# Optimization experiments

Hardware: AMD Instinct MI355X
Metric: run time of the kernel (lower is better)

Reference implementation:

```python
import jax, jax.numpy as jnp
import numpy as np
from jax import lax

WS = 8   # window size
NH = 8   # num heads
EPS = 1e-5  # BatchNorm eps (eval mode, running mean=0 var=1)

def _rel_pos_index(ws):
    coords = np.stack(np.meshgrid(np.arange(ws), np.arange(ws), indexing='ij'))
    cf = coords.reshape(2, -1)
    rel = (cf[:, :, None] - cf[:, None, :]).transpose(1, 2, 0).astype(np.int64)
    rel[..., 0] += ws - 1
    rel[..., 1] += ws - 1
    rel[..., 0] *= 2 * ws - 1
    return rel.sum(-1)  # [ws*ws, ws*ws]

REL_IDX = _rel_pos_index(WS)

def conv2d(x, w, b=None, pad=0, groups=1):
    y = lax.conv_general_dilated(x, w, (1, 1), [(pad, pad), (pad, pad)],
                                 dimension_numbers=('NCHW', 'OIHW', 'NCHW'),
                                 feature_group_count=groups)
    if b is not None:
        y = y + b[None, :, None, None]
    return y

def bn(x, g, b):
    # eval-mode BatchNorm with running_mean=0, running_var=1
    scale = g / np.float32(np.sqrt(1.0 + EPS))
    return x * scale[None, :, None, None] + b[None, :, None, None]

def avgpool(x, kh, kw, ph, pw):
    # PyTorch AvgPool2d: zero padding, count_include_pad=True -> divide by kernel size
    s = lax.reduce_window(x, 0.0, lax.add, (1, 1, kh, kw), (1, 1, 1, 1),
                          [(0, 0), (0, 0), (ph, ph), (pw, pw)])
    return s / (kh * kw)

def setup_inputs() -> dict:
    key = jax.random.key(0)
    ks = jax.random.split(key, 8)
    C = 256
    x = jax.random.normal(ks[0], (8, C, 128, 128), dtype=jnp.float32)
    qkv_w = jax.random.normal(ks[1], (3 * C, C, 1, 1), dtype=jnp.float32) * 0.05
    qkv_b = jnp.zeros((3 * C,), jnp.float32)
    local_w = jax.random.normal(ks[2], (C, C // NH, 3, 3), dtype=jnp.float32) * 0.05
    local_b = jnp.zeros((C,), jnp.float32)
    rpb_table = jax.random.normal(ks[3], ((2 * WS - 1) ** 2, NH), dtype=jnp.float32) * 0.02
    proj_dw_w = jax.random.normal(ks[4], (C, 1, 3, 3), dtype=jnp.float32) * 0.05
    proj_dw_b = jnp.zeros((C,), jnp.float32)
    proj_pw_w = jax.random.normal(ks[5], (C, C, 1, 1), dtype=jnp.float32) * 0.05
    proj_pw_b = jnp.zeros((C,), jnp.float32)
    return {
        'x': x, 'qkv_w': qkv_w, 'qkv_b': qkv_b,
        'local_w': local_w, 'local_b': local_b,
        'local_bn_g': jnp.ones((C,), jnp.float32), 'local_bn_b': jnp.zeros((C,), jnp.float32),
        'rpb_table': rpb_table,
        'proj_dw_w': proj_dw_w, 'proj_dw_b': proj_dw_b,
        'proj_bn_g': jnp.ones((C,), jnp.float32), 'proj_bn_b': jnp.zeros((C,), jnp.float32),
        'proj_pw_w': proj_pw_w, 'proj_pw_b': proj_pw_b,
    }

def reference(x, qkv_w, qkv_b, local_w, local_b, local_bn_g, local_bn_b,
              rpb_table, proj_dw_w, proj_dw_b, proj_bn_g, proj_bn_b,
              proj_pw_w, proj_pw_b):
    B, C, H, W = x.shape
    hd = C // NH
    scale = hd ** -0.5
    # local branch: grouped 3x3 conv (groups=num_heads) + BN + ReLU
    local = jax.nn.relu(bn(conv2d(x, local_w, local_b, pad=1, groups=NH),
                           local_bn_g, local_bn_b))
    # H, W divisible by WS -> self.pad (reflect) is a no-op
    qkv = conv2d(x, qkv_w, qkv_b)  # [B, 3C, H, W]
    Hh, Ww = H // WS, W // WS
    # 'b (qkv h d) (hh ws1) (ww ws2) -> qkv (b hh ww) h (ws1 ws2) d'
    qkv = qkv.reshape(B, 3, NH, hd, Hh, WS, Ww, WS)
    qkv = qkv.transpose(1, 0, 4, 6, 2, 5, 7, 3).reshape(3, B * Hh * Ww, NH, WS * WS, hd)
    q, k, v = qkv[0], qkv[1], qkv[2]
    dots = jnp.einsum('bhid,bhjd->bhij', q, k) * scale  # [Bwin, NH, 64, 64]
    bias = rpb_table[REL_IDX.reshape(-1)].reshape(WS * WS, WS * WS, NH).transpose(2, 0, 1)
    attn = jax.nn.softmax(dots + bias[None], axis=-1)
    out = jnp.einsum('bhij,bhjd->bhid', attn, v)
    # '(b hh ww) h (ws1 ws2) d -> b (h d) (hh ws1) (ww ws2)'
    out = out.reshape(B, Hh, Ww, NH, WS, WS, hd).transpose(0, 3, 6, 1, 4, 2, 5).reshape(B, C, H, W)
    # asymmetric avg-pool fusion with reflect pre-pad
    ax = avgpool(jnp.pad(out, ((0, 0), (0, 0), (0, 1), (0, 0)), mode='reflect'),
                 WS, 1, WS // 2 - 1, 0)
    ay = avgpool(jnp.pad(out, ((0, 0), (0, 0), (0, 0), (0, 1)), mode='reflect'),
                 1, WS, 0, WS // 2 - 1)
    out = ax + ay + local
    # pad_out: reflect (0,1,0,1)
    out = jnp.pad(out, ((0, 0), (0, 0), (0, 1), (0, 1)), mode='reflect')
    # SeparableConvBN proj: depthwise 3x3 -> BN -> pointwise 1x1
    out = conv2d(out, proj_dw_w, proj_dw_b, pad=1, groups=C)
    out = bn(out, proj_bn_g, proj_bn_b)
    out = conv2d(out, proj_pw_w, proj_pw_b)
    return out[:, :, :H, :W]
```

## Files before the change

### kernel.cpp

```cpp
#include <hip/hip_runtime.h>
#include <cstddef>

#define C_ 256
#define H_ 128
#define W_ 128
#define HW_ 16384
#define NH_ 8
#define NWIN_ 256
#define EPS_ 1e-5f

typedef short s16x8 __attribute__((ext_vector_type(8)));
typedef float f32x4 __attribute__((ext_vector_type(4)));

__device__ inline void bf16_split(float f, short& h, short& l) {
  unsigned u = __float_as_uint(f);
  unsigned hb = (u + 0x7FFFu + ((u >> 16) & 1u)) >> 16;
  float hf = __uint_as_float(hb << 16);
  h = (short)hb;
  float r = f - hf;
  unsigned v = __float_as_uint(r);
  unsigned lb = (v + 0x7FFFu + ((v >> 16) & 1u)) >> 16;
  l = (short)lb;
}

__global__ __launch_bounds__(256) void k1_qkv_mfma(
    const float* __restrict__ xb, const float* __restrict__ wq,
    const float* __restrict__ bias, float* __restrict__ qkv_s) {
  __shared__ short s_a[2][128][40];
  __shared__ short s_b[2][128][40];
  const int tid = threadIdx.x;
  const int y   = blockIdx.x;
  const int oc0 = blockIdx.y * 128;

  const int lane = tid & 63;
  const int wid  = tid >> 6;
  const int m0w = (wid >> 1) * 64;
  const int n0w = (wid & 1) * 64;

  f32x4 acc[4][4];
#pragma unroll
  for (int i = 0; i < 4; ++i)
#pragma unroll
    for (int j = 0; j < 4; ++j) acc[i][j] = f32x4{0.f, 0.f, 0.f, 0.f};

  const int pcol = tid & 127;
  const int kq0  = tid >> 7;

  for (int k0 = 0; k0 < 256; k0 += 32) {
#pragma unroll
    for (int i = 0; i < 4; ++i) {
      const int ff = tid + i * 256;
      const int row = ff >> 3;
      const int c4 = ff & 7;
      const float4 w4 = *reinterpret_cast<const float4*>(
          &wq[(size_t)(oc0 + row) * 256 + k0 + c4 * 4]);
      short h0, h1, h2, h3, l0, l1, l2, l3;
      bf16_split(w4.x, h0, l0);
      bf16_split(w4.y, h1, l1);
      bf16_split(w4.z, h2, l2);
      bf16_split(w4.w, h3, l3);
      *reinterpret_cast<short4*>(&s_a[0][row][c4 * 4]) = make_short4(h0, h1, h2, h3);
      *reinterpret_cast<short4*>(&s_a[1][row][c4 * 4]) = make_short4(l0, l1, l2, l3);
    }
#pragma unroll
    for (int it = 0; it < 4; ++it) {
      const int kq = kq0 * 4 + it;
      short h[4], l[4];
#pragma unroll
      for (int e = 0; e < 4; ++e) {
        const float v = xb[(size_t)(k0 + kq * 4 + e) * HW_ + y * W_ + pcol];
        bf16_split(v, h[e], l[e]);
      }
      *reinterpret_cast<short4*>(&s_b[0][pcol][kq * 4]) = make_short4(h[0], h[1], h[2], h[3]);
      *reinterpret_cast<short4*>(&s_b[1][pcol][kq * 4]) = make_short4(l[0], l[1], l[2], l[3]);
    }
    __syncthreads();

    const int mr = lane & 15;
    const int kg = (lane >> 4) * 8;
    s16x8 ah[4], al[4], bh[4], bl[4];
#pragma unroll
    for (int fm = 0; fm < 4; ++fm) {
      ah[fm] = *reinterpret_cast<const s16x8*>(&s_a[0][m0w + fm * 16 + mr][kg]);
      al[fm] = *reinterpret_cast<const s16x8*>(&s_a[1][m0w + fm * 16 + mr][kg]);
    }
#pragma unroll
    for (int fn = 0; fn < 4; ++fn) {
      bh[fn] = *reinterpret_cast<const s16x8*>(&s_b[0][n0w + fn * 16 + mr][kg]);
      bl[fn] = *reinterpret_cast<const s16x8*>(&s_b[1][n0w + fn * 16 + mr][kg]);
    }
#pragma unroll
    for (int fm = 0; fm < 4; ++fm)
#pragma unroll
      for (int fn = 0; fn < 4; ++fn) {
        acc[fm][fn] = __builtin_amdgcn_mfma_f32_16x16x32_bf16(
            ah[fm], bh[fn], acc[fm][fn], 0, 0, 0);
        acc[fm][fn] = __builtin_amdgcn_mfma_f32_16x16x32_bf16(
            ah[fm], bl[fn], acc[fm][fn], 0, 0, 0);
        acc[fm][fn] = __builtin_amdgcn_mfma_f32_16x16x32_bf16(
            al[fm], bh[fn], acc[fm][fn], 0, 0, 0);
      }
    __syncthreads();
  }

  const int mr4 = (lane >> 4) * 4;
  const int nn  = lane & 15;
  const int hh = y >> 3, ws1 = y & 7;
#pragma unroll
  for (int fm = 0; fm < 4; ++fm) {
    const int oc = oc0 + m0w + fm * 16 + mr4;
    const float4 b4 = *reinterpret_cast<const float4*>(&bias[oc]);
    const int qkvi = oc >> 8;
    const int head = (oc >> 5) & 7;
    const int d0 = oc & 31;
#pragma unroll
    for (int fn = 0; fn < 4; ++fn) {
      const int x = n0w + fn * 16 + nn;
      const int win = hh * 16 + (x >> 3);
      const int pos = ws1 * 8 + (x & 7);
      const size_t addr =
          ((((size_t)qkvi * NWIN_ + win) * NH_ + head) * 64 + pos) * 32 + d0;
      float4 v;
      v.x = acc[fm][fn].x + b4.x;
      v.y = acc[fm][fn].y + b4.y;
      v.z = acc[fm][fn].z + b4.z;
      v.w = acc[fm][fn].w + b4.w;
      *reinterpret_cast<float4*>(&qkv_s[addr]) = v;
    }
  }
}

__global__ __launch_bounds__(256) void k2_local(
    const float* __restrict__ x, const float* __restrict__ lw,
    const float* __restrict__ lb, const float* __restrict__ bng,
    const float* __restrict__ bnb, float* __restrict__ local_buf) {
  __shared__ float xt[18 * 35];
  __shared__ float wl[288];
  const int tid = threadIdx.x;
  const int g = blockIdx.y;
  const int bb = blockIdx.z;
  const int ty0 = (blockIdx.x >> 2) * 16;
  const int tx0 = (blockIdx.x & 3) * 32;
  const int py = tid >> 4;
  const int px = (tid & 15) * 2;
  const float* xb = x + (size_t)bb * C_ * HW_;

  float acc0[32], acc1[32];
#pragma unroll
  for (int oc = 0; oc < 32; ++oc) { acc0[oc] = 0.f; acc1[oc] = 0.f; }

  for (int ic = 0; ic < 32; ++ic) {
    __syncthreads();
    const float* xp = xb + (size_t)(g * 32 + ic) * HW_;
    for (int i = tid; i < 18 * 34; i += 256) {
      const int r = i / 34, cc = i % 34;
      const int gy = ty0 + r - 1, gx = tx0 + cc - 1;
      float v = 0.f;
      if (gy >= 0 && gy < H_ && gx >= 0 && gx < W_) v = xp[gy * W_ + gx];
      xt[r * 35 + cc] = v;
    }
    for (int i = tid; i < 288; i += 256) {
      const int oc = i / 9, k = i % 9;
      wl[i] = lw[((size_t)(g * 32 + oc) * 32 + ic) * 9 + k];
    }
    __syncthreads();
    float nb[3][4];
#pragma unroll
    for (int dy = 0; dy < 3; ++dy)
#pragma unroll
      for (int dx = 0; dx < 4; ++dx) nb[dy][dx] = xt[(py + dy) * 35 + px + dx];
#pragma unroll
    for (int oc = 0; oc < 32; ++oc) {
      const float* wp = &wl[oc * 9];
      float s0 = 0.f, s1 = 0.f;
#pragma unroll
      for (int dy = 0; dy < 3; ++dy)
#pragma unroll
        for (int dx = 0; dx < 3; ++dx) {
          const float wv = wp[dy * 3 + dx];
          s0 = fmaf(nb[dy][dx], wv, s0);
          s1 = fmaf(nb[dy][dx + 1], wv, s1);
        }
      acc0[oc] += s0;
      acc1[oc] += s1;
    }
  }

  const int gy = ty0 + py;
#pragma unroll
  for (int oc = 0; oc < 32; ++oc) {
    const int c = g * 32 + oc;
    const float scale = bng[c] / sqrtf(1.0f + EPS_);
    const float cb = lb[c], sb = bnb[c];
    const float v0 = fmaxf(fmaf(acc0[oc] + cb, scale, sb), 0.f);
    const float v1 = fmaxf(fmaf(acc1[oc] + cb, scale, sb), 0.f);
    *reinterpret_cast<float2*>(
        &local_buf[((size_t)(bb * C_ + c)) * HW_ + gy * W_ + tx0 + px]) =
        make_float2(v0, v1);
  }
}

__global__ __launch_bounds__(128) void k3_attn(
    const float* __restrict__ qkv_s, const float* __restrict__ rpb,
    float* __restrict__ attn_s) {
  __shared__ float kvs[2][2][64 * 32];
  __shared__ float rpb_s[225 * 8];
  const int tid = threadIdx.x;
  const int wid = tid >> 6, lane = tid & 63;
  const int pid = blockIdx.x * 2 + wid;
  const int win = pid >> 3, h = pid & 7;
  const int hh = win >> 4, ww = win & 15;

  for (int i = tid; i < 225 * 8; i += 128) rpb_s[i] = rpb[i];

  const size_t qbase = (((size_t)0 * NWIN_ + win) * NH_ + h) * 2048;
  const size_t kbase = (((size_t)1 * NWIN_ + win) * NH_ + h) * 2048;
  const size_t vbase = (((size_t)2 * NWIN_ + win) * NH_ + h) * 2048;

  float* Kl = kvs[wid][0];
  float* Vl = kvs[wid][1];
#pragma unroll
  for (int r = 0; r < 8; ++r) {
    const int e = r * 256 + lane * 4;
    *reinterpret_cast<float4*>(&Kl[e]) =
        *reinterpret_cast<const float4*>(&qkv_s[kbase + e]);
    *reinterpret_cast<float4*>(&Vl[e]) =
        *reinterpret_cast<const float4*>(&qkv_s[vbase + e]);
  }
  float4 qreg[8];
#pragma unroll
  for (int dd = 0; dd < 8; ++dd)
    qreg[dd] = *reinterpret_cast<const float4*>(&qkv_s[qbase + lane * 32 + dd * 4]);

  __syncthreads();

  float s[64];
#pragma unroll
  for (int j = 0; j < 64; ++j) {
    const float* kr = &Kl[j * 32];
    float sj = 0.f;
#pragma unroll
    for (int dd = 0; dd < 8; ++dd) {
      const float4 kv = *reinterpret_cast<const float4*>(&kr[dd * 4]);
      sj = fmaf(qreg[dd].x, kv.x, sj);
      sj = fmaf(qreg[dd].y, kv.y, sj);
      sj = fmaf(qreg[dd].z, kv.z, sj);
      sj = fmaf(qreg[dd].w, kv.w, sj);
    }
    s[j] = sj;
  }

  const float scale = 0.17677669529663687f;
  const int r1 = lane >> 3, c1 = lane & 7;
  float m = -1e30f;
#pragma unroll
  for (int j = 0; j < 64; ++j) {
    const int jr = j >> 3, jc = j & 7;
    const int idx = (r1 - jr + 7) * 15 + (c1 - jc + 7);
    s[j] = fmaf(s[j], scale, rpb_s[idx * 8 + h]);
    m = fmaxf(m, s[j]);
  }
  float sum = 0.f;
#pragma unroll
  for (int j = 0; j < 64; ++j) {
    s[j] = __expf(s[j] - m);
    sum += s[j];
  }
  const float inv = 1.0f / sum;

  float o[32];
#pragma unroll
  for (int d = 0; d < 32; ++d) o[d] = 0.f;
#pragma unroll
  for (int j = 0; j < 64; ++j) {
    const float pj = s[j] * inv;
    const float* vr = &Vl[j * 32];
#pragma unroll
    for (int dd = 0; dd < 8; ++dd) {
      const float4 vv = *reinterpret_cast<const float4*>(&vr[dd * 4]);
      o[dd * 4 + 0] = fmaf(pj, vv.x, o[dd * 4 + 0]);
      o[dd * 4 + 1] = fmaf(pj, vv.y, o[dd * 4 + 1]);
      o[dd * 4 + 2] = fmaf(pj, vv.z, o[dd * 4 + 2]);
      o[dd * 4 + 3] = fmaf(pj, vv.w, o[dd * 4 + 3]);
    }
  }

  const int yy = hh * 8 + r1, xx = ww * 8 + c1;
  const size_t obase = ((size_t)(h * 32) * H_ + yy) * W_ + xx;
#pragma unroll
  for (int d = 0; d < 32; ++d) attn_s[obase + (size_t)d * HW_] = o[d];
}

__global__ __launch_bounds__(256) void k4_pool(
    const float* __restrict__ attn_s, float* __restrict__ localpool) {
  const int bid = blockIdx.x;
  const int c = bid >> 6;
  const int rp = bid & 63;
  const int i = rp * 2 + (threadIdx.x >> 7);
  const int j = threadIdx.x & 127;
  const float* ap = attn_s + (size_t)c * HW_;
  float sx = 0.f;
#pragma unroll
  for (int dr = -3; dr <= 4; ++dr) {
    int r = i + dr;
    if (r < 0 || r > 128) continue;
    if (r == 128) r = 126;
    sx += ap[r * W_ + j];
  }
  float sy = 0.f;
#pragma unroll
  for (int dc = -3; dc <= 4; ++dc) {
    int cc = j + dc;
    if (cc < 0 || cc > 128) continue;
    if (cc == 128) cc = 126;
    sy += ap[i * W_ + cc];
  }
  const size_t idx = (size_t)c * HW_ + i * W_ + j;
  localpool[idx] = (sx + sy) * 0.125f + localpool[idx];
}

__global__ __launch_bounds__(256) void k5_dw(
    const float* __restrict__ pool, const float* __restrict__ dww,
    const float* __restrict__ dwb, const float* __restrict__ bng,
    const float* __restrict__ bnb, float* __restrict__ dwout) {
  const int bid = blockIdx.x;
  const int c = bid >> 6;
  const int rp = bid & 63;
  const int i = rp * 2 + (threadIdx.x >> 7);
  const int j = threadIdx.x & 127;
  const float* pp = pool + (size_t)c * HW_;
  const float* wp = dww + c * 9;
  float acc = 0.f;
#pragma unroll
  for (int dy = 0; dy < 3; ++dy) {
    int r = i + dy - 1;
    if (r < 0) continue;
    if (r == 128) r = 126;
#pragma unroll
    for (int dx = 0; dx < 3; ++dx) {
      int cc = j + dx - 1;
      if (cc < 0) continue;
      if (cc == 128) cc = 126;
      acc = fmaf(wp[dy * 3 + dx], pp[r * W_ + cc], acc);
    }
  }
  const float scale = bng[c] / sqrtf(1.0f + EPS_);
  dwout[(size_t)c * HW_ + i * W_ + j] = fmaf(acc + dwb[c], scale, bnb[c]);
}

__global__ __launch_bounds__(256) void k6_pw_gemm(
    const float* __restrict__ xin, const float* __restrict__ wp,
    const float* __restrict__ bias, float* __restrict__ outb) {
  __shared__ float s_w[32][64];
  __shared__ float s_x[32][64];
  const int tid = threadIdx.x;
  const int tx = tid & 15, ty = tid >> 4;
  const int p0 = blockIdx.x * 64;
  const int oc0 = blockIdx.y * 64;

  const int m = tid >> 2;
  const int kg = (tid & 3) * 4;
  const int kkld = tid >> 4;
  const int cg = (tid & 15) * 4;

  float acc[4][4];
#pragma unroll
  for (int i = 0; i < 4; ++i)
#pragma unroll
    for (int j = 0; j < 4; ++j) acc[i][j] = 0.f;

  for (int k0 = 0; k0 < 256; k0 += 32) {
    const float4 w0 = *reinterpret_cast<const float4*>(
        &wp[(size_t)(oc0 + m) * 256 + k0 + kg]);
    const float4 w1 = *reinterpret_cast<const float4*>(
        &wp[(size_t)(oc0 + m) * 256 + k0 + kg + 16]);
    const float4 x0 = *reinterpret_cast<const float4*>(
        &xin[(size_t)(k0 + kkld) * HW_ + p0 + cg]);
    const float4 x1 = *reinterpret_cast<const float4*>(
        &xin[(size_t)(k0 + kkld + 16) * HW_ + p0 + cg]);
    s_w[kg + 0][m] = w0.x;  s_w[kg + 1][m] = w0.y;
    s_w[kg + 2][m] = w0.z;  s_w[kg + 3][m] = w0.w;
    s_w[kg + 16][m] = w1.x; s_w[kg + 17][m] = w1.y;
    s_w[kg + 18][m] = w1.z; s_w[kg + 19][m] = w1.w;
    *reinterpret_cast<float4*>(&s_x[kkld][cg]) = x0;
    *reinterpret_cast<float4*>(&s_x[kkld + 16][cg]) = x1;
    __syncthreads();
#pragma unroll
    for (int kk = 0; kk < 32; ++kk) {
      const float4 a = *reinterpret_cast<const float4*>(&s_w[kk][ty * 4]);
      const float4 bv = *reinterpret_cast<const float4*>(&s_x[kk][tx * 4]);
      acc[0][0] = fmaf(a.x, bv.x, acc[0][0]);
      acc[0][1] = fmaf(a.x, bv.y, acc[0][1]);
      acc[0][2] = fmaf(a.x, bv.z, acc[0][2]);
      acc[0][3] = fmaf(a.x, bv.w, acc[0][3]);
      acc[1][0] = fmaf(a.y, bv.x, acc[1][0]);
      acc[1][1] = fmaf(a.y, bv.y, acc[1][1]);
      acc[1][2] = fmaf(a.y, bv.z, acc[1][2]);
      acc[1][3] = fmaf(a.y, bv.w, acc[1][3]);
      acc[2][0] = fmaf(a.z, bv.x, acc[2][0]);
      acc[2][1] = fmaf(a.z, bv.y, acc[2][1]);
      acc[2][2] = fmaf(a.z, bv.z, acc[2][2]);
      acc[2][3] = fmaf(a.z, bv.w, acc[2][3]);
      acc[3][0] = fmaf(a.w, bv.x, acc[3][0]);
      acc[3][1] = fmaf(a.w, bv.y, acc[3][1]);
      acc[3][2] = fmaf(a.w, bv.z, acc[3][2]);
      acc[3][3] = fmaf(a.w, bv.w, acc[3][3]);
    }
    __syncthreads();
  }

#pragma unroll
  for (int i = 0; i < 4; ++i) {
    const int oc = oc0 + ty * 4 + i;
    const float bo = bias[oc];
    float4 v;
    v.x = acc[i][0] + bo;
    v.y = acc[i][1] + bo;
    v.z = acc[i][2] + bo;
    v.w = acc[i][3] + bo;
    *reinterpret_cast<float4*>(&outb[(size_t)oc * HW_ + p0 + tx * 4]) = v;
  }
}

extern "C" void kernel_launch(void* const* d_in, const int* in_sizes, int n_in,
                              void* d_out, int out_size, void* d_ws, size_t ws_size,
                              hipStream_t stream) {
  const float* x          = (const float*)d_in[0];
  const float* qkv_w      = (const float*)d_in[1];
  const float* qkv_b      = (const float*)d_in[2];
  const float* local_w    = (const float*)d_in[3];
  const float* local_b    = (const float*)d_in[4];
  const float* local_bn_g = (const float*)d_in[5];
  const float* local_bn_b = (const float*)d_in[6];
  const float* rpb        = (const float*)d_in[7];
  const float* proj_dw_w  = (const float*)d_in[8];
  const float* proj_dw_b  = (const float*)d_in[9];
  const float* proj_bn_g  = (const float*)d_in[10];
  const float* proj_bn_b  = (const float*)d_in[11];
  const float* proj_pw_w  = (const float*)d_in[12];
  const float* proj_pw_b  = (const float*)d_in[13];
  float* out = (float*)d_out;
  float* ws = (float*)d_ws;

  const size_t CHW = (size_t)C_ * HW_;
  const size_t NEED_BATCHED  = (8 + 3 + 1) * CHW * 4;
  const size_t NEED_FALLBACK = (3 + 2) * CHW * 4;

  if (ws_size >= NEED_BATCHED) {
    float* local_all = ws;
    float* qkv_s     = ws + 8 * CHW;
    float* attn_s    = qkv_s + 3 * CHW;

    k2_local<<<dim3(32, NH_, 8), 256, 0, stream>>>(
        x, local_w, local_b, local_bn_g, local_bn_b, local_all);
    for (int bb = 0; bb < 8; ++bb) {
      const float* xb = x + (size_t)bb * CHW;
      float* outb = out + (size_t)bb * CHW;
      float* local_s = local_all + (size_t)bb * CHW;
      k1_qkv_mfma<<<dim3(128, 6), 256, 0, stream>>>(xb, qkv_w, qkv_b, qkv_s);
      k3_attn<<<dim3(1024), 128, 0, stream>>>(qkv_s, rpb, attn_s);
      k4_pool<<<dim3(C_ * 64), 256, 0, stream>>>(attn_s, local_s);
      k5_dw<<<dim3(C_ * 64), 256, 0, stream>>>(local_s, proj_dw_w, proj_dw_b,
                                               proj_bn_g, proj_bn_b, attn_s);
      k6_pw_gemm<<<dim3(256, 4), 256, 0, stream>>>(attn_s, proj_pw_w, proj_pw_b, outb);
    }
  } else {
    if (ws_size < NEED_FALLBACK) return;
    float* qkv_s   = ws;
    float* attn_s  = ws + 3 * CHW;
    float* local_s = attn_s + CHW;
    for (int bb = 0; bb < 8; ++bb) {
      const float* xb = x + (size_t)bb * CHW;
      float* outb = out + (size_t)bb * CHW;
      k1_qkv_mfma<<<dim3(128, 6), 256, 0, stream>>>(xb, qkv_w, qkv_b, qkv_s);
      k2_local<<<dim3(32, NH_, 1), 256, 0, stream>>>(
          xb, local_w, local_b, local_bn_g, local_bn_b, local_s);
      k3_attn<<<dim3(1024), 128, 0, stream>>>(qkv_s, rpb, attn_s);
      k4_pool<<<dim3(C_ * 64), 256, 0, stream>>>(attn_s, local_s);
      k5_dw<<<dim3(C_ * 64), 256, 0, stream>>>(local_s, proj_dw_w, proj_dw_b,
                                               proj_bn_g, proj_bn_b, attn_s);
      k6_pw_gemm<<<dim3(256, 4), 256, 0, stream>>>(attn_s, proj_pw_w, proj_pw_b, outb);
    }
  }
}
```

Measured before the change: 2.138 ms.

## Move grouped 3x3 local conv and pointwise projection onto split-bf16 MFMA

Replaces the scalar-FMA grouped 3x3 convolution with an MFMA implicit GEMM over the nine taps. Weights are pre-split into bf16 hi/lo parts by a small prep kernel, and input rows are staged in LDS as hi/lo bf16 with an XOR swizzle. The fp32 pointwise projection GEMM is also rewritten to use 3-pass split-bf16 MFMA on 128x128 tiles. This targets the scalar FP32 compute cost of both convolutions, at the cost of some precision (no lo*lo term) and extra conversion work. The small-workspace fallback path is dropped.

```diff
diff --git a/kernel.cpp b/kernel.cpp
--- a/kernel.cpp
+++ b/kernel.cpp
@@ -130,74 +130,109 @@
   }
 }
 
-__global__ __launch_bounds__(256) void k2_local(
-    const float* __restrict__ x, const float* __restrict__ lw,
+__global__ __launch_bounds__(256) void k2_wt(
+    const float* __restrict__ lw, short* __restrict__ WT) {
+  const int i = blockIdx.x * 256 + threadIdx.x;
+  if (i >= 73728) return;
+  const int g = i / 9216;
+  const int rem = i % 9216;
+  const int tau = rem / 1024;
+  const int oc = (rem >> 5) & 31;
+  const int ic = rem & 31;
+  const float w = lw[((size_t)(g * 32 + oc) * 32 + ic) * 9 + tau];
+  short h, l;
+  bf16_split(w, h, l);
+  WT[((g * 9 + tau) * 2 + 0) * 1024 + oc * 32 + ic] = h;
+  WT[((g * 9 + tau) * 2 + 1) * 1024 + oc * 32 + ic] = l;
+}
+
+__global__ __launch_bounds__(256) void k2_mfma(
+    const float* __restrict__ x, const short* __restrict__ WT,
     const float* __restrict__ lb, const float* __restrict__ bng,
     const float* __restrict__ bnb, float* __restrict__ local_buf) {
-  __shared__ float xt[18 * 35];
-  __shared__ float wl[288];
+  __shared__ short xt[3][132][64];
   const int tid = threadIdx.x;
+  const int y = blockIdx.x;
   const int g = blockIdx.y;
   const int bb = blockIdx.z;
-  const int ty0 = (blockIdx.x >> 2) * 16;
-  const int tx0 = (blockIdx.x & 3) * 32;
-  const int py = tid >> 4;
-  const int px = (tid & 15) * 2;
-  const float* xb = x + (size_t)bb * C_ * HW_;
-
-  float acc0[32], acc1[32];
-#pragma unroll
-  for (int oc = 0; oc < 32; ++oc) { acc0[oc] = 0.f; acc1[oc] = 0.f; }
-
-  for (int ic = 0; ic < 32; ++ic) {
-    __syncthreads();
-    const float* xp = xb + (size_t)(g * 32 + ic) * HW_;
-    for (int i = tid; i < 18 * 34; i += 256) {
-      const int r = i / 34, cc = i % 34;
-      const int gy = ty0 + r - 1, gx = tx0 + cc - 1;
-      float v = 0.f;
-      if (gy >= 0 && gy < H_ && gx >= 0 && gx < W_) v = xp[gy * W_ + gx];
-      xt[r * 35 + cc] = v;
-    }
-    for (int i = tid; i < 288; i += 256) {
-      const int oc = i / 9, k = i % 9;
-      wl[i] = lw[((size_t)(g * 32 + oc) * 32 + ic) * 9 + k];
-    }
-    __syncthreads();
-    float nb[3][4];
-#pragma unroll
-    for (int dy = 0; dy < 3; ++dy)
-#pragma unroll
-      for (int dx = 0; dx < 4; ++dx) nb[dy][dx] = xt[(py + dy) * 35 + px + dx];
-#pragma unroll
-    for (int oc = 0; oc < 32; ++oc) {
-      const float* wp = &wl[oc * 9];
-      float s0 = 0.f, s1 = 0.f;
-#pragma unroll
-      for (int dy = 0; dy < 3; ++dy)
-#pragma unroll
-        for (int dx = 0; dx < 3; ++dx) {
-          const float wv = wp[dy * 3 + dx];
-          s0 = fmaf(nb[dy][dx], wv, s0);
-          s1 = fmaf(nb[dy][dx + 1], wv, s1);
-        }
-      acc0[oc] += s0;
-      acc1[oc] += s1;
-    }
-  }
-
-  const int gy = ty0 + py;
-#pragma unroll
-  for (int oc = 0; oc < 32; ++oc) {
-    const int c = g * 32 + oc;
-    const float scale = bng[c] / sqrtf(1.0f + EPS_);
-    const float cb = lb[c], sb = bnb[c];
-    const float v0 = fmaxf(fmaf(acc0[oc] + cb, scale, sb), 0.f);
-    const float v1 = fmaxf(fmaf(acc1[oc] + cb, scale, sb), 0.f);
-    *reinterpret_cast<float2*>(
-        &local_buf[((size_t)(bb * C_ + c)) * HW_ + gy * W_ + tx0 + px]) =
-        make_float2(v0, v1);
-  }
+
+  for (int i = tid; i < 12480; i += 256) {
+    const int r = i / 4160;
+    const int rem = i - r * 4160;
+    const int ic = rem / 130;
+    const int px = rem - ic * 130 - 1;
+    const int gy = y + r - 1;
+    float v = 0.f;
+    if (gy >= 0 && gy < H_ && px >= 0 && px < W_)
+      v = x[(((size_t)(bb * C_ + g * 32 + ic)) * H_ + gy) * W_ + px];
+    short h, l;
+    bf16_split(v, h, l);
+    const int slot = px + 1;
+    const int sw = (slot & 7) * 8;
+    xt[r][slot][(ic) ^ sw] = h;
+    xt[r][slot][(32 + ic) ^ sw] = l;
+  }
+  __syncthreads();
+
+  const int lane = tid & 63;
+  const int wid = tid >> 6;
+  const int px0w = wid * 32;
+  const int mr = lane & 15;
+  const int kg = (lane >> 4) * 8;
+
+  f32x4 acc[2][2];
+#pragma unroll
+  for (int i = 0; i < 2; ++i)
+#pragma unroll
+    for (int j = 0; j < 2; ++j) acc[i][j] = f32x4{0.f, 0.f, 0.f, 0.f};
+
+#pragma unroll
+  for (int tau = 0; tau < 9; ++tau) {
+    const int dy = tau / 3;
+    const int dx = tau % 3;
+    const int wt0 = ((g * 9 + tau) * 2) * 1024;
+    s16x8 ah[2], al[2], bh[2], bl[2];
+#pragma unroll
+    for (int fm = 0; fm < 2; ++fm) {
+      ah[fm] = *reinterpret_cast<const s16x8*>(&WT[wt0 + (fm * 16 + mr) * 32 + kg]);
+      al[fm] = *reinterpret_cast<const s16x8*>(&WT[wt0 + 1024 + (fm * 16 + mr) * 32 + kg]);
+    }
+#pragma unroll
+    for (int fn = 0; fn < 2; ++fn) {
+      const int slot = px0w + fn * 16 + mr + dx;
+      const int sw = (slot & 7) * 8;
+      bh[fn] = *reinterpret_cast<const s16x8*>(&xt[dy][slot][(kg) ^ sw]);
+      bl[fn] = *reinterpret_cast<const s16x8*>(&xt[dy][slot][(32 + kg) ^ sw]);
+    }
+#pragma unroll
+    for (int fm = 0; fm < 2; ++fm)
+#pragma unroll
+      for (int fn = 0; fn < 2; ++fn) {
+        acc[fm][fn] = __builtin_amdgcn_mfma_f32_16x16x32_bf16(
+            ah[fm], bh[fn], acc[fm][fn], 0, 0, 0);
+        acc[fm][fn] = __builtin_amdgcn_mfma_f32_16x16x32_bf16(
+            ah[fm], bl[fn], acc[fm][fn], 0, 0, 0);
+        acc[fm][fn] = __builtin_amdgcn_mfma_f32_16x16x32_bf16(
+            al[fm], bh[fn], acc[fm][fn], 0, 0, 0);
+      }
+  }
+
+  const int mr4 = (lane >> 4) * 4;
+  const float inv_s = 1.0f / sqrtf(1.0f + EPS_);
+#pragma unroll
+  for (int fm = 0; fm < 2; ++fm)
+#pragma unroll
+    for (int r = 0; r < 4; ++r) {
+      const int c = g * 32 + fm * 16 + mr4 + r;
+      const float scale = bng[c] * inv_s;
+      const float cb = lb[c], sb = bnb[c];
+#pragma unroll
+      for (int fn = 0; fn < 2; ++fn) {
+        const int px = px0w + fn * 16 + mr;
+        const float val = fmaxf(fmaf(acc[fm][fn][r] + cb, scale, sb), 0.f);
+        local_buf[(((size_t)(bb * C_ + c)) * H_ + y) * W_ + px] = val;
+      }
+    }
 }
 
 __global__ __launch_bounds__(128) void k3_attn(
@@ -348,77 +383,101 @@
   dwout[(size_t)c * HW_ + i * W_ + j] = fmaf(acc + dwb[c], scale, bnb[c]);
 }
 
-__global__ __launch_bounds__(256) void k6_pw_gemm(
-    const float* __restrict__ xin, const float* __restrict__ wp,
+__global__ __launch_bounds__(256) void k6_pw_mfma(
+    const float* __restrict__ xin, const float* __restrict__ wq,
     const float* __restrict__ bias, float* __restrict__ outb) {
-  __shared__ float s_w[32][64];
-  __shared__ float s_x[32][64];
+  __shared__ short s_a[2][128][40];
+  __shared__ short s_b[2][128][40];
   const int tid = threadIdx.x;
-  const int tx = tid & 15, ty = tid >> 4;
-  const int p0 = blockIdx.x * 64;
-  const int oc0 = blockIdx.y * 64;
-
-  const int m = tid >> 2;
-  const int kg = (tid & 3) * 4;
-  const int kkld = tid >> 4;
-  const int cg = (tid & 15) * 4;
-
-  float acc[4][4];
+  const int y   = blockIdx.x;
+  const int oc0 = blockIdx.y * 128;
+
+  const int lane = tid & 63;
+  const int wid  = tid >> 6;
+  const int m0w = (wid >> 1) * 64;
+  const int n0w = (wid & 1) * 64;
+
+  f32x4 acc[4][4];
 #pragma unroll
   for (int i = 0; i < 4; ++i)
 #pragma unroll
-    for (int j = 0; j < 4; ++j) acc[i][j] = 0.f;
+    for (int j = 0; j < 4; ++j) acc[i][j] = f32x4{0.f, 0.f, 0.f, 0.f};
+
+  const int pcol = tid & 127;
+  const int kq0  = tid >> 7;
 
   for (int k0 = 0; k0 < 256; k0 += 32) {
-    const float4 w0 = *reinterpret_cast<const float4*>(
-        &wp[(size_t)(oc0 + m) * 256 + k0 + kg]);
-    const float4 w1 = *reinterpret_cast<const float4*>(
-        &wp[(size_t)(oc0 + m) * 256 + k0 + kg + 16]);
-    const float4 x0 = *reinterpret_cast<const float4*>(
-        &xin[(size_t)(k0 + kkld) * HW_ + p0 + cg]);
-    const float4 x1 = *reinterpret_cast<const float4*>(
-        &xin[(size_t)(k0 + kkld + 16) * HW_ + p0 + cg]);
-    s_w[kg + 0][m] = w0.x;  s_w[kg + 1][m] = w0.y;
-    s_w[kg + 2][m] = w0.z;  s_w[kg + 3][m] = w0.w;
-    s_w[kg + 16][m] = w1.x; s_w[kg + 17][m] = w1.y;
-    s_w[kg + 18][m] = w1.z; s_w[kg + 19][m] = w1.w;
-    *reinterpret_cast<float4*>(&s_x[kkld][cg]) = x0;
-    *reinterpret_cast<float4*>(&s_x[kkld + 16][cg]) = x1;
+#pragma unroll
+    for (int i = 0; i < 4; ++i) {
+      const int ff = tid + i * 256;
+      const int row = ff >> 3;
+      const int c4 = ff & 7;
+      const float4 w4 = *reinterpret_cast<const float4*>(
+          &wq[(size_t)(oc0 + row) * 256 + k0 + c4 * 4]);
+      short h0, h1, h2, h3, l0, l1, l2, l3;
+      bf16_split(w4.x, h0, l0);
+      bf16_split(w4.y, h1, l1);
+      bf16_split(w4.z, h2, l2);
+      bf16_split(w4.w, h3, l3);
+      *reinterpret_cast<short4*>(&s_a[0][row][c4 * 4]) = make_short4(h0, h1, h2, h3);
+      *reinterpret_cast<short4*>(&s_a[1][row][c4 * 4]) = make_short4(l0, l1, l2, l3);
+    }
+#pragma unroll
+    for (int it = 0; it < 4; ++it) {
+      const int kq = kq0 * 4 + it;
+      short h[4], l[4];
+#pragma unroll
+      for (int e = 0; e < 4; ++e) {
+        const float v = xin[(size_t)(k0 + kq * 4 + e) * HW_ + y * W_ + pcol];
+        bf16_split(v, h[e], l[e]);
+      }
+      *reinterpret_cast<short4*>(&s_b[0][pcol][kq * 4]) = make_short4(h[0], h[1], h[2], h[3]);
+      *reinterpret_cast<short4*>(&s_b[1][pcol][kq * 4]) = make_short4(l[0], l[1], l[2], l[3]);
+    }
     __syncthreads();
-#pragma unroll
-    for (int kk = 0; kk < 32; ++kk) {
-      const float4 a = *reinterpret_cast<const float4*>(&s_w[kk][ty * 4]);
-      const float4 bv = *reinterpret_cast<const float4*>(&s_x[kk][tx * 4]);
-      acc[0][0] = fmaf(a.x, bv.x, acc[0][0]);
-      acc[0][1] = fmaf(a.x, bv.y, acc[0][1]);
-      acc[0][2] = fmaf(a.x, bv.z, acc[0][2]);
-      acc[0][3] = fmaf(a.x, bv.w, acc[0][3]);
-      acc[1][0] = fmaf(a.y, bv.x, acc[1][0]);
-      acc[1][1] = fmaf(a.y, bv.y, acc[1][1]);
-      acc[1][2] = fmaf(a.y, bv.z, acc[1][2]);
-      acc[1][3] = fmaf(a.y, bv.w, acc[1][3]);
-      acc[2][0] = fmaf(a.z, bv.x, acc[2][0]);
-      acc[2][1] = fmaf(a.z, bv.y, acc[2][1]);
-      acc[2][2] = fmaf(a.z, bv.z, acc[2][2]);
-      acc[2][3] = fmaf(a.z, bv.w, acc[2][3]);
-      acc[3][0] = fmaf(a.w, bv.x, acc[3][0]);
-      acc[3][1] = fmaf(a.w, bv.y, acc[3][1]);
-      acc[3][2] = fmaf(a.w, bv.z, acc[3][2]);
-      acc[3][3] = fmaf(a.w, bv.w, acc[3][3]);
-    }
+
+    const int mr = lane & 15;
+    const int kg = (lane >> 4) * 8;
+    s16x8 ah[4], al[4], bh[4], bl[4];
+#pragma unroll
+    for (int fm = 0; fm < 4; ++fm) {
+      ah[fm] = *reinterpret_cast<const s16x8*>(&s_a[0][m0w + fm * 16 + mr][kg]);
+      al[fm] = *reinterpret_cast<const s16x8*>(&s_a[1][m0w + fm * 16 + mr][kg]);
+    }
+#pragma unroll
+    for (int fn = 0; fn < 4; ++fn) {
+      bh[fn] = *reinterpret_cast<const s16x8*>(&s_b[0][n0w + fn * 16 + mr][kg]);
+      bl[fn] = *reinterpret_cast<const s16x8*>(&s_b[1][n0w + fn * 16 + mr][kg]);
+    }
+#pragma unroll
+    for (int fm = 0; fm < 4; ++fm)
+#pragma unroll
+      for (int fn = 0; fn < 4; ++fn) {
+        acc[fm][fn] = __builtin_amdgcn_mfma_f32_16x16x32_bf16(
+            ah[fm], bh[fn], acc[fm][fn], 0, 0, 0);
+        acc[fm][fn] = __builtin_amdgcn_mfma_f32_16x16x32_bf16(
+            ah[fm], bl[fn], acc[fm][fn], 0, 0, 0);
+        acc[fm][fn] = __builtin_amdgcn_mfma_f32_16x16x32_bf16(
+            al[fm], bh[fn], acc[fm][fn], 0, 0, 0);
+      }
     __syncthreads();
   }
 
-#pragma unroll
-  for (int i = 0; i < 4; ++i) {
-    const int oc = oc0 + ty * 4 + i;
-    const float bo = bias[oc];
-    float4 v;
-    v.x = acc[i][0] + bo;
-    v.y = acc[i][1] + bo;
-    v.z = acc[i][2] + bo;
-    v.w = acc[i][3] + bo;
-    *reinterpret_cast<float4*>(&outb[(size_t)oc * HW_ + p0 + tx * 4]) = v;
+  const int mr4 = (lane >> 4) * 4;
+  const int nn  = lane & 15;
+#pragma unroll
+  for (int fm = 0; fm < 4; ++fm) {
+    const int ocb = oc0 + m0w + fm * 16 + mr4;
+#pragma unroll
+    for (int r = 0; r < 4; ++r) {
+      const int oc = ocb + r;
+      const float bo = bias[oc];
+#pragma unroll
+      for (int fn = 0; fn < 4; ++fn) {
+        const int px = n0w + fn * 16 + nn;
+        outb[(size_t)oc * HW_ + y * W_ + px] = acc[fm][fn][r] + bo;
+      }
+    }
   }
 }
 
@@ -443,43 +502,27 @@
   float* ws = (float*)d_ws;
 
   const size_t CHW = (size_t)C_ * HW_;
-  const size_t NEED_BATCHED  = (8 + 3 + 1) * CHW * 4;
-  const size_t NEED_FALLBACK = (3 + 2) * CHW * 4;
-
-  if (ws_size >= NEED_BATCHED) {
-    float* local_all = ws;
-    float* qkv_s     = ws + 8 * CHW;
-    float* attn_s    = qkv_s + 3 * CHW;
-
-    k2_local<<<dim3(32, NH_, 8), 256, 0, stream>>>(
-        x, local_w, local_b, local_bn_g, local_bn_b, local_all);
-    for (int bb = 0; bb < 8; ++bb) {
-      const float* xb = x + (size_t)bb * CHW;
-      float* outb = out + (size_t)bb * CHW;
-      float* local_s = local_all + (size_t)bb * CHW;
-      k1_qkv_mfma<<<dim3(128, 6), 256, 0, stream>>>(xb, qkv_w, qkv_b, qkv_s);
-      k3_attn<<<dim3(1024), 128, 0, stream>>>(qkv_s, rpb, attn_s);
-      k4_pool<<<dim3(C_ * 64), 256, 0, stream>>>(attn_s, local_s);
-      k5_dw<<<dim3(C_ * 64), 256, 0, stream>>>(local_s, proj_dw_w, proj_dw_b,
-                                               proj_bn_g, proj_bn_b, attn_s);
-      k6_pw_gemm<<<dim3(256, 4), 256, 0, stream>>>(attn_s, proj_pw_w, proj_pw_b, outb);
-    }
-  } else {
-    if (ws_size < NEED_FALLBACK) return;
-    float* qkv_s   = ws;
-    float* attn_s  = ws + 3 * CHW;
-    float* local_s = attn_s + CHW;
-    for (int bb = 0; bb < 8; ++bb) {
-      const float* xb = x + (size_t)bb * CHW;
-      float* outb = out + (size_t)bb * CHW;
-      k1_qkv_mfma<<<dim3(128, 6), 256, 0, stream>>>(xb, qkv_w, qkv_b, qkv_s);
-      k2_local<<<dim3(32, NH_, 1), 256, 0, stream>>>(
-          xb, local_w, local_b, local_bn_g, local_bn_b, local_s);
-      k3_attn<<<dim3(1024), 128, 0, stream>>>(qkv_s, rpb, attn_s);
-      k4_pool<<<dim3(C_ * 64), 256, 0, stream>>>(attn_s, local_s);
-      k5_dw<<<dim3(C_ * 64), 256, 0, stream>>>(local_s, proj_dw_w, proj_dw_b,
-                                               proj_bn_g, proj_bn_b, attn_s);
-      k6_pw_gemm<<<dim3(256, 4), 256, 0, stream>>>(attn_s, proj_pw_w, proj_pw_b, outb);
-    }
-  }
-}
+  const size_t NEED = 12 * CHW * 4;
+  if (ws_size < NEED) return;
+
+  float* local_all = ws;
+  float* qkv_s     = ws + 8 * CHW;
+  float* attn_s    = qkv_s + 3 * CHW;
+  short* WT = (short*)qkv_s;
+
+  k2_wt<<<dim3(288), 256, 0, stream>>>(local_w, WT);
+  k2_mfma<<<dim3(128, 8, 8), 256, 0, stream>>>(
+      x, WT, local_b, local_bn_g, local_bn_b, local_all);
+
+  for (int bb = 0; bb < 8; ++bb) {
+    const float* xb = x + (size_t)bb * CHW;
+    float* outb = out + (size_t)bb * CHW;
+    float* local_s = local_all + (size_t)bb * CHW;
+    k1_qkv_mfma<<<dim3(128, 6), 256, 0, stream>>>(xb, qkv_w, qkv_b, qkv_s);
+    k3_attn<<<dim3(1024), 128, 0, stream>>>(qkv_s, rpb, attn_s);
+    k4_pool<<<dim3(C_ * 64), 256, 0, stream>>>(attn_s, local_s);
+    k5_dw<<<dim3(C_ * 64), 256, 0, stream>>>(local_s, proj_dw_w, proj_dw_b,
+                                             proj_bn_g, proj_bn_b, attn_s);
+    k6_pw_mfma<<<dim3(128, 2), 256, 0, stream>>>(attn_s, proj_pw_w, proj_pw_b, outb);
+  }
+}
```

Result: faster. 1.914 ms (-10.4%).
